# Kernel optimization log

Hardware: AMD Instinct MI355X
Metric: run time of the kernel (lower is better)

Reference implementation:

```python
import jax, jax.numpy as jnp
import numpy as np

D_K = 64

def setup_inputs() -> dict:
    key = jax.random.key(0)
    kq, kk, kv, km = jax.random.split(key, 4)
    B, H, S, D = 8, 12, 1024, D_K
    Q = jax.random.normal(kq, (B, H, S, D), dtype=jnp.float32)
    K = jax.random.normal(kk, (B, H, S, D), dtype=jnp.float32)
    V = jax.random.normal(kv, (B, H, S, D), dtype=jnp.float32)
    # boolean mask: True = masked out (as used by masked_fill_)
    attn_mask = jax.random.randint(km, (B, H, S, S), 0, 2) == 1
    return {"Q": Q, "K": K, "V": V, "attn_mask": attn_mask}

def reference(Q, K, V, attn_mask):
    # scores: [B, H, S, S]
    scale = 1.0 / np.sqrt(D_K).astype(np.float32)
    scores = jnp.einsum('bhqd,bhkd->bhqk', Q, K) * scale
    scores = jnp.where(attn_mask, jnp.float32(-1e9), scores)
    attn = jax.nn.softmax(scores, axis=-1)
    context = jnp.einsum('bhqk,bhkd->bhqd', attn, V)
    return (context, attn)
```

## Files before the change

### kernel.cpp

```cpp
#include <hip/hip_runtime.h>

#define S_LEN  1024
#define D_KK   64
#define N_HEAD 96
#define BQ     16
#define TK     128
#define NT_QK  (S_LEN / TK)
#define CHK    128
#define NCH    (S_LEN / CHK)
#define KSTR   129
#define QSTR   132
#define VSTR   68

__global__ __launch_bounds__(256, 2) void attn_fused_kernel(
    const float* __restrict__ Qg, const float* __restrict__ Kg,
    const float* __restrict__ Vg, const int* __restrict__ maskg,
    float* __restrict__ attng, float* __restrict__ ctxg)
{
    __shared__ float smA[CHK * VSTR];
    __shared__ float smB[BQ * QSTR];

    const int t     = threadIdx.x;
    const int lane  = t & 63;
    const int wave  = t >> 6;
    const int head  = blockIdx.y;
    const int q0    = blockIdx.x * BQ;
    const int rbase = wave << 2;

    {
        const int r  = t >> 4;
        const int d0 = (t & 15) << 2;
        const float4 qv = *(const float4*)(Qg + ((size_t)head * S_LEN + q0 + r) * D_KK + d0);
        smB[r * QSTR + d0 + 0] = qv.x;
        smB[r * QSTR + d0 + 1] = qv.y;
        smB[r * QSTR + d0 + 2] = qv.z;
        smB[r * QSTR + d0 + 3] = qv.w;
    }

    float s[4][16];
    #pragma unroll
    for (int r = 0; r < 4; ++r)
        #pragma unroll
        for (int j = 0; j < 16; ++j) s[r][j] = 0.f;

    #pragma unroll
    for (int kt_i = 0; kt_i < NT_QK; ++kt_i) {
        __syncthreads();
        {
            const int d0 = (t & 15) << 2;
            const int kb = t >> 4;
            #pragma unroll
            for (int c = 0; c < TK / 16; ++c) {
                const int kl = c * 16 + kb;
                const float4 kv = *(const float4*)(Kg + ((size_t)head * S_LEN + kt_i * TK + kl) * D_KK + d0);
                smA[(d0 + 0) * KSTR + kl] = kv.x;
                smA[(d0 + 1) * KSTR + kl] = kv.y;
                smA[(d0 + 2) * KSTR + kl] = kv.z;
                smA[(d0 + 3) * KSTR + kl] = kv.w;
            }
        }
        __syncthreads();

        #pragma unroll
        for (int d0 = 0; d0 < D_KK; d0 += 4) {
            float4 qv[4];
            #pragma unroll
            for (int r = 0; r < 4; ++r)
                qv[r] = *(const float4*)(&smB[(rbase + r) * QSTR + d0]);
            #pragma unroll
            for (int dd = 0; dd < 4; ++dd) {
                const float k0v = smA[(d0 + dd) * KSTR + lane];
                const float k1v = smA[(d0 + dd) * KSTR + lane + 64];
                #pragma unroll
                for (int r = 0; r < 4; ++r) {
                    const float qd = (&qv[r].x)[dd];
                    s[r][2 * kt_i + 0] = fmaf(qd, k0v, s[r][2 * kt_i + 0]);
                    s[r][2 * kt_i + 1] = fmaf(qd, k1v, s[r][2 * kt_i + 1]);
                }
            }
        }
    }

    #pragma unroll
    for (int r = 0; r < 4; ++r) {
        const int q = q0 + rbase + r;
        const int*  mrow = maskg + ((size_t)head * S_LEN + q) * S_LEN;
        float*      arow = attng + ((size_t)head * S_LEN + q) * S_LEN;
        float m = -3.0e38f;
        #pragma unroll
        for (int j = 0; j < 16; ++j) {
            const int mk = __builtin_nontemporal_load(&mrow[lane + 64 * j]);
            float v = s[r][j] * 0.125f;
            if (mk) v = -1.0e9f;
            s[r][j] = v;
            m = fmaxf(m, v);
        }
        #pragma unroll
        for (int off = 32; off >= 1; off >>= 1)
            m = fmaxf(m, __shfl_xor(m, off, 64));
        float l = 0.0f;
        #pragma unroll
        for (int j = 0; j < 16; ++j) {
            s[r][j] = __expf(s[r][j] - m);
            l += s[r][j];
        }
        #pragma unroll
        for (int off = 32; off >= 1; off >>= 1)
            l += __shfl_xor(l, off, 64);
        const float inv = 1.0f / l;
        #pragma unroll
        for (int j = 0; j < 16; ++j) {
            s[r][j] *= inv;
            __builtin_nontemporal_store(s[r][j], &arow[lane + 64 * j]);
        }
    }

    float acc0 = 0.f, acc1 = 0.f, acc2 = 0.f, acc3 = 0.f;
    const int qr = lane >> 4;
    const int tx = lane & 15;

    #pragma unroll
    for (int c = 0; c < NCH; ++c) {
        __syncthreads();
        #pragma unroll
        for (int p_ = 0; p_ < 8; ++p_) {
            const int i  = t + 256 * p_;
            const int k  = i >> 4;
            const int d0 = (i & 15) << 2;
            const float4 v = *(const float4*)(Vg + ((size_t)head * S_LEN + c * CHK + k) * D_KK + d0);
            *(float4*)(&smA[k * VSTR + d0]) = v;
        }
        #pragma unroll
        for (int r = 0; r < 4; ++r) {
            smB[(rbase + r) * QSTR + lane]      = s[r][2 * c + 0];
            smB[(rbase + r) * QSTR + 64 + lane] = s[r][2 * c + 1];
        }
        __syncthreads();

        const float* prow = &smB[(rbase + qr) * QSTR];
        #pragma unroll 4
        for (int k4 = 0; k4 < CHK / 4; ++k4) {
            const float4 a4 = *(const float4*)(prow + 4 * k4);
            #pragma unroll
            for (int e = 0; e < 4; ++e) {
                const float  a = (&a4.x)[e];
                const float4 v = *(const float4*)(&smA[(4 * k4 + e) * VSTR + (tx << 2)]);
                acc0 = fmaf(a, v.x, acc0);
                acc1 = fmaf(a, v.y, acc1);
                acc2 = fmaf(a, v.z, acc2);
                acc3 = fmaf(a, v.w, acc3);
            }
        }
    }

    float4 o; o.x = acc0; o.y = acc1; o.z = acc2; o.w = acc3;
    *(float4*)(ctxg + ((size_t)head * S_LEN + q0 + rbase + qr) * D_KK + (tx << 2)) = o;
}

extern "C" void kernel_launch(void* const* d_in, const int* in_sizes, int n_in,
                              void* d_out, int out_size, void* d_ws, size_t ws_size,
                              hipStream_t stream) {
    const float* Q    = (const float*)d_in[0];
    const float* K    = (const float*)d_in[1];
    const float* V    = (const float*)d_in[2];
    const int*   mask = (const int*)d_in[3];

    float* ctx  = (float*)d_out;
    float* attn = ctx + (size_t)N_HEAD * S_LEN * D_KK;

    dim3 grid(S_LEN / BQ, N_HEAD);
    attn_fused_kernel<<<grid, 256, 0, stream>>>(Q, K, V, mask, attn, ctx);
}
```

Measured before the change: 1.186 ms.

## Split PV over key rows per thread with register tile and cross-wave reduction

Restructures the P·V stage. Each thread now owns 8 keys per chunk and 4 output dims for all 16 query rows, instead of one query row by 4 dims over all 128 keys. This reuses each loaded V float4 across 16 rows and cuts LDS reads per FMA. Partial sums are then reduced with shuffles across key groups inside a wave and through shared memory across waves. The cost is 64 accumulator registers per thread, which may pressure occupancy under launch_bounds(256,2), plus extra reduction syncs.

```diff
diff --git a/kernel.cpp b/kernel.cpp
--- a/kernel.cpp
+++ b/kernel.cpp
@@ -9,16 +9,17 @@
 #define CHK    128
 #define NCH    (S_LEN / CHK)
 #define KSTR   129
-#define QSTR   132
+#define QSTR   68
 #define VSTR   68
+#define PSTR   136
 
 __global__ __launch_bounds__(256, 2) void attn_fused_kernel(
     const float* __restrict__ Qg, const float* __restrict__ Kg,
     const float* __restrict__ Vg, const int* __restrict__ maskg,
     float* __restrict__ attng, float* __restrict__ ctxg)
 {
-    __shared__ float smA[CHK * VSTR];
-    __shared__ float smB[BQ * QSTR];
+    __shared__ __align__(16) float smA[CHK * VSTR];
+    __shared__ __align__(16) float smB[BQ * PSTR];
 
     const int t     = threadIdx.x;
     const int lane  = t & 63;
@@ -115,9 +116,14 @@
         }
     }
 
-    float acc0 = 0.f, acc1 = 0.f, acc2 = 0.f, acc3 = 0.f;
-    const int qr = lane >> 4;
-    const int tx = lane & 15;
+    const int tk = t >> 4;
+    const int td = t & 15;
+
+    float acc[16][4];
+    #pragma unroll
+    for (int r = 0; r < 16; ++r)
+        #pragma unroll
+        for (int d = 0; d < 4; ++d) acc[r][d] = 0.f;
 
     #pragma unroll
     for (int c = 0; c < NCH; ++c) {
@@ -132,29 +138,60 @@
         }
         #pragma unroll
         for (int r = 0; r < 4; ++r) {
-            smB[(rbase + r) * QSTR + lane]      = s[r][2 * c + 0];
-            smB[(rbase + r) * QSTR + 64 + lane] = s[r][2 * c + 1];
-        }
-        __syncthreads();
-
-        const float* prow = &smB[(rbase + qr) * QSTR];
-        #pragma unroll 4
-        for (int k4 = 0; k4 < CHK / 4; ++k4) {
-            const float4 a4 = *(const float4*)(prow + 4 * k4);
-            #pragma unroll
-            for (int e = 0; e < 4; ++e) {
-                const float  a = (&a4.x)[e];
-                const float4 v = *(const float4*)(&smA[(4 * k4 + e) * VSTR + (tx << 2)]);
-                acc0 = fmaf(a, v.x, acc0);
-                acc1 = fmaf(a, v.y, acc1);
-                acc2 = fmaf(a, v.z, acc2);
-                acc3 = fmaf(a, v.w, acc3);
+            smB[(rbase + r) * PSTR + lane]      = s[r][2 * c + 0];
+            smB[(rbase + r) * PSTR + 64 + lane] = s[r][2 * c + 1];
+        }
+        __syncthreads();
+
+        #pragma unroll
+        for (int e = 0; e < 2; ++e) {
+            float4 v4[4];
+            #pragma unroll
+            for (int i = 0; i < 4; ++i)
+                v4[i] = *(const float4*)(&smA[(8 * tk + 4 * e + i) * VSTR + (td << 2)]);
+            #pragma unroll
+            for (int r = 0; r < 16; ++r) {
+                const float4 p4 = *(const float4*)(&smB[r * PSTR + 8 * tk + 4 * e]);
+                #pragma unroll
+                for (int i = 0; i < 4; ++i) {
+                    const float p = (&p4.x)[i];
+                    acc[r][0] = fmaf(p, v4[i].x, acc[r][0]);
+                    acc[r][1] = fmaf(p, v4[i].y, acc[r][1]);
+                    acc[r][2] = fmaf(p, v4[i].z, acc[r][2]);
+                    acc[r][3] = fmaf(p, v4[i].w, acc[r][3]);
+                }
             }
         }
     }
 
-    float4 o; o.x = acc0; o.y = acc1; o.z = acc2; o.w = acc3;
-    *(float4*)(ctxg + ((size_t)head * S_LEN + q0 + rbase + qr) * D_KK + (tx << 2)) = o;
+    #pragma unroll
+    for (int r = 0; r < 16; ++r)
+        #pragma unroll
+        for (int d = 0; d < 4; ++d) {
+            acc[r][d] += __shfl_xor(acc[r][d], 16, 64);
+            acc[r][d] += __shfl_xor(acc[r][d], 32, 64);
+        }
+    __syncthreads();
+    {
+        const int qg  = lane >> 4;
+        const int tdw = lane & 15;
+        #pragma unroll
+        for (int rr = 0; rr < 4; ++rr) {
+            const int r = 4 * qg + rr;
+            float4 a; a.x = acc[r][0]; a.y = acc[r][1]; a.z = acc[r][2]; a.w = acc[r][3];
+            *(float4*)(&smA[(wave * 256 + r * 16 + tdw) * 4]) = a;
+        }
+    }
+    __syncthreads();
+    {
+        float4 o = *(const float4*)(&smA[(0 * 256 + t) * 4]);
+        #pragma unroll
+        for (int w = 1; w < 4; ++w) {
+            const float4 p = *(const float4*)(&smA[(w * 256 + t) * 4]);
+            o.x += p.x; o.y += p.y; o.z += p.z; o.w += p.w;
+        }
+        *(float4*)(ctxg + ((size_t)head * S_LEN + q0 + (t >> 4)) * D_KK + ((t & 15) << 2)) = o;
+    }
 }
 
 extern "C" void kernel_launch(void* const* d_in, const int* in_sizes, int n_in,
```

New measurement: 1.589 ms. 1.34x slower.
